# Optimization experiments

Measured on AMD Instinct MI355X. Metric: run time of the kernel, lower is better.

Reference implementation:

```python
import math
import jax, jax.numpy as jnp
import numpy as np

B, S, D, H, HD = 32, 512, 768, 12, 64
K, ST = 2, 2  # pooling kernel / stride
NEG = jnp.float32(-10000.0)


def _alibi_slopes(n):
    def p2(m):
        start = 2 ** (-(2 ** (-(math.log2(m) - 3))))
        return [start * start ** i for i in range(m)]
    if math.log2(n).is_integer():
        return p2(n)
    c = 2 ** math.floor(math.log2(n))
    return p2(c) + _alibi_slopes(2 * c)[0::2][: n - c]


def _sum_pool(x, k, s, out_len):
    # x: [B, L, C]; ceil_mode sum-pool over axis 1 (zero padded on the right)
    pad = (out_len - 1) * s + k - x.shape[1]
    if pad > 0:
        x = jnp.pad(x, ((0, 0), (0, pad), (0, 0)))
    win = x[:, jnp.arange(out_len)[:, None] * s + jnp.arange(k)]  # [B, out, k, C]
    return win.sum(axis=2)


def setup_inputs() -> dict:
    key = jax.random.key(0)
    k1, k2, k3 = jax.random.split(key, 3)
    hidden_states = jax.random.normal(k1, (B, S, D), dtype=jnp.float32)
    lengths = jax.random.randint(k2, (B,), 128, S + 1)
    attention_mask = jnp.arange(S)[None, :] < lengths[:, None]  # bool [B,S]
    Wqkv_w = jax.random.normal(k3, (3 * D, D), dtype=jnp.float32) * 0.02
    Wqkv_b = jnp.zeros((3 * D,), dtype=jnp.float32)
    return {"hidden_states": hidden_states, "attention_mask": attention_mask,
            "Wqkv_w": Wqkv_w, "Wqkv_b": Wqkv_b}


def reference(hidden_states, attention_mask, Wqkv_w, Wqkv_b):
    b, s = attention_mask.shape
    qkv = hidden_states @ Wqkv_w.T + Wqkv_b  # [B,S,3D]
    qkv = qkv.reshape(b, s, 3, H, HD)        # '(t h d)' split order
    q = qkv[:, :, 0]                          # [B,S,H,HD]
    k = qkv[:, :, 1].transpose(0, 2, 1, 3)    # [B,H,S,HD]
    v = qkv[:, :, 2].transpose(0, 2, 1, 3)

    # MaskedAvgPool1d on queries (flattened heads), ceil_mode sum-pool / count
    kk = min(K, s)
    out_len = -(-(max(0, s - kk)) // ST) + 1
    q_flat = q.reshape(b, s, H * HD)
    q_flat = jnp.where(attention_mask[:, :, None], q_flat, 0.0)
    norm = _sum_pool(attention_mask.astype(jnp.float32)[:, :, None], kk, ST, out_len)  # [B,out,1]
    new_mask = norm[..., 0] != 0
    norm = jnp.where(norm == 0, 1.0, norm)
    q_pool = _sum_pool(q_flat, kk, ST, out_len) / norm  # [B,out,D]
    q = q_pool.reshape(b, out_len, H, HD).transpose(0, 2, 1, 3)  # [B,H,out,HD]

    # bias: 0 where (new_mask_q & mask_k), else -10000; plus ALiBi
    pair = new_mask[:, :, None] & attention_mask[:, None, :]  # [B,out,S]
    bias = jnp.where(pair, 0.0, NEG)[:, None, :, :]           # [B,1,out,S]
    rel = jnp.abs(jnp.arange(s)[None, :] - jnp.arange(out_len)[:, None])  # [out,S]
    slopes = jnp.asarray(_alibi_slopes(H), dtype=jnp.float32)
    alibi = slopes[:, None, None] * (-rel.astype(jnp.float32))  # [H,out,S]
    scores = jnp.einsum('bhqd,bhkd->bhqk', q, k) / math.sqrt(HD) + bias + alibi[None]
    attn = jax.nn.softmax(scores, axis=-1)
    out = jnp.einsum('bhqk,bhkd->bhqd', attn, v)  # [B,H,out,HD]
    out = out.transpose(0, 2, 1, 3).reshape(b, out_len, H * HD)
    return out, new_mask
```

## Files before the change

kernel.cpp:

```cpp
#include <hip/hip_runtime.h>

#define BB 32
#define SS 512
#define DD 768
#define HH 12
#define HDIM 64
#define OL 256
#define NQKV 2304
#define GM (BB*SS)

#define NEG2 (-14426.9504089f)

typedef __bf16 bf16_t;
typedef bf16_t bf16x8 __attribute__((ext_vector_type(8)));
typedef float f32x4 __attribute__((ext_vector_type(4)));
typedef unsigned short u16x8 __attribute__((ext_vector_type(8)));

__device__ __forceinline__ unsigned short f2bf(float f) {
  unsigned u = __float_as_uint(f);
  u = u + 0x7FFFu + ((u >> 16) & 1u);
  return (unsigned short)(u >> 16);
}
__device__ __forceinline__ float b2f(unsigned short s) {
  return __uint_as_float(((unsigned)s) << 16);
}

__global__ void conv_f32_bf16(const float* __restrict__ in,
                              unsigned short* __restrict__ out, int n4) {
  int i = blockIdx.x * blockDim.x + threadIdx.x;
  if (i >= n4) return;
  float4 v = ((const float4*)in)[i];
  ushort4 o;
  o.x = f2bf(v.x); o.y = f2bf(v.y); o.z = f2bf(v.z); o.w = f2bf(v.w);
  ((ushort4*)out)[i] = o;
}

__global__ void prep_mask(const void* __restrict__ mraw,
                          float* __restrict__ kbias,
                          float* __restrict__ invn,
                          unsigned char* __restrict__ nmask,
                          float* __restrict__ out_nm) {
  int b = blockIdx.x, t = threadIdx.x;
  const unsigned char* mb = (const unsigned char*)mraw;
  bool isbyte = (mb[1] != 0);
  int idx = b * SS + t;
  int mv = isbyte ? (int)(mb[idx] != 0) : (int)(((const int*)mraw)[idx] != 0);
  kbias[idx] = mv ? 0.f : NEG2;
  if (t < OL) {
    int i0 = b * SS + 2 * t, i1 = i0 + 1;
    int m0 = isbyte ? (int)(mb[i0] != 0) : (int)(((const int*)mraw)[i0] != 0);
    int m1 = isbyte ? (int)(mb[i1] != 0) : (int)(((const int*)mraw)[i1] != 0);
    int n = m0 + m1;
    invn[b * OL + t] = (n > 0) ? 1.f / (float)n : 1.f;
    nmask[b * OL + t] = (n > 0) ? 1 : 0;
    out_nm[b * OL + t] = (n > 0) ? 1.f : 0.f;
  }
}

__global__ __launch_bounds__(512, 2) void gemm_qkv(
    const unsigned short* __restrict__ A,
    const unsigned short* __restrict__ Bt,
    const float* __restrict__ bias,
    unsigned short* __restrict__ Kbuf,
    unsigned short* __restrict__ qp,
    unsigned short* __restrict__ vT,
    const float* __restrict__ kbias,
    const float* __restrict__ invn) {
  __shared__ __align__(16) char smem[147456];

  const int t = threadIdx.x;
  const int lane = t & 63;
  const int w = t >> 6;
  const int wm = w >> 2;
  const int wn = w & 3;
  const int fr = lane & 15, hi = lane >> 4;

  const int p = blockIdx.x;
  const int l = (p & 7) * 144 + (p >> 3);
  const int m0 = (l / 9) * 128;
  const int n0 = (l % 9) * 256;
  const int b = m0 >> 9;
  const int s0 = m0 & 511;

  f32x4 acc[4][4] = {};

  const int sr8 = lane >> 3;
  const int sx8 = ((lane & 7) ^ sr8) * 8;
  const int wq = __builtin_amdgcn_readfirstlane(w);
  const unsigned short* aS = A + (size_t)(m0 + wq * 16 + sr8) * DD + sx8;
  const unsigned short* bS = Bt + (size_t)(n0 + wq * 32 + sr8) * DD + sx8;

#define GLOAD(SRC, DST)                                                        \
  __builtin_amdgcn_global_load_lds(                                           \
      (const __attribute__((address_space(1))) unsigned int*)(SRC),           \
      (__attribute__((address_space(3))) unsigned int*)(DST), 16, 0, 0)

#define STG_A(KT, SB, Q) GLOAD(aS + (size_t)(8 * (Q)) * DD + (KT) * 64,        \
                               (SB) + (wq * 16 + 8 * (Q)) * 128)
#define STG_B(KT, SB, Q) GLOAD(bS + (size_t)(8 * (Q)) * DD + (KT) * 64,        \
                               (SB) + 16384 + (wq * 32 + 8 * (Q)) * 128)
#define STG_H1(KT, SB) do { STG_A(KT, SB, 0); STG_A(KT, SB, 1); STG_B(KT, SB, 0); } while (0)
#define STG_H2(KT, SB) do { STG_B(KT, SB, 1); STG_B(KT, SB, 2); STG_B(KT, SB, 3); } while (0)

#define SBAR()                                                                 \
  do {                                                                         \
    __builtin_amdgcn_sched_barrier(0);                                         \
    __builtin_amdgcn_s_barrier();                                              \
    __builtin_amdgcn_sched_barrier(0);                                         \
  } while (0)

#define MFMA16(AF, BF)                                                         \
  do {                                                                         \
    asm volatile("s_waitcnt lgkmcnt(0)" ::: "memory");                          \
    __builtin_amdgcn_sched_barrier(0);                                         \
    __builtin_amdgcn_s_setprio(1);                                             \
    _Pragma("unroll")                                                          \
    for (int mf_ = 0; mf_ < 4; ++mf_)                                          \
      _Pragma("unroll")                                                        \
      for (int nf_ = 0; nf_ < 4; ++nf_)                                        \
        acc[mf_][nf_] = __builtin_amdgcn_mfma_f32_16x16x32_bf16(               \
            (AF)[mf_], (BF)[nf_], acc[mf_][nf_], 0, 0, 0);                     \
    __builtin_amdgcn_s_setprio(0);                                             \
  } while (0)

  const int cb0 = (hi * 16) ^ ((fr & 7) << 4);
  const int cb1 = (64 + hi * 16) ^ ((fr & 7) << 4);
  const int arow = (wm * 64 + fr) * 128;
  const int brow = 16384 + (wn * 64 + fr) * 128;

  STG_H1(0, smem); STG_H2(0, smem);
  STG_H1(1, smem + 49152); STG_H2(1, smem + 49152);

  int se = 0;
#pragma unroll
  for (int it = 0; it < 6; ++it) {
    char* sE = smem + se * 49152;
    char* sO = smem + (se == 2 ? 0 : se + 1) * 49152;
    char* dE = smem + (se == 0 ? 2 : se - 1) * 49152;
    char* dO = sE;
    const int ke = 2 * it + 2, ko = 2 * it + 3;

    bf16x8 af[4], bf[4];

    asm volatile("s_waitcnt vmcnt(6)" ::: "memory");
    SBAR();
#pragma unroll
    for (int f = 0; f < 4; ++f) af[f] = *(const bf16x8*)(sE + arow + f * 2048 + cb0);
#pragma unroll
    for (int f = 0; f < 4; ++f) bf[f] = *(const bf16x8*)(sE + brow + f * 2048 + cb0);
    if (it < 5) STG_H1(ke, dE);
    MFMA16(af, bf);

    SBAR();
#pragma unroll
    for (int f = 0; f < 4; ++f) af[f] = *(const bf16x8*)(sE + arow + f * 2048 + cb1);
#pragma unroll
    for (int f = 0; f < 4; ++f) bf[f] = *(const bf16x8*)(sE + brow + f * 2048 + cb1);
    if (it < 5) STG_H2(ke, dE);
    MFMA16(af, bf);

    if (it < 5) {
      asm volatile("s_waitcnt vmcnt(6)" ::: "memory");
    } else {
      asm volatile("s_waitcnt vmcnt(0)" ::: "memory");
    }
    SBAR();
#pragma unroll
    for (int f = 0; f < 4; ++f) af[f] = *(const bf16x8*)(sO + arow + f * 2048 + cb0);
#pragma unroll
    for (int f = 0; f < 4; ++f) bf[f] = *(const bf16x8*)(sO + brow + f * 2048 + cb0);
    if (it < 5) STG_H1(ko, dO);
    MFMA16(af, bf);

    SBAR();
#pragma unroll
    for (int f = 0; f < 4; ++f) af[f] = *(const bf16x8*)(sO + arow + f * 2048 + cb1);
#pragma unroll
    for (int f = 0; f < 4; ++f) bf[f] = *(const bf16x8*)(sO + brow + f * 2048 + cb1);
    if (it < 5) STG_H2(ko, dO);
    MFMA16(af, bf);

    se = (se + 2) % 3;
  }
#undef STG_A
#undef STG_B
#undef STG_H1
#undef STG_H2
#undef MFMA16
#undef SBAR
#undef GLOAD

  const int nt = n0 / 768;
  if (nt == 1) {
#pragma unroll
    for (int nf = 0; nf < 4; ++nf) {
      const int nc = wn * 64 + nf * 16 + fr;
      const float bvs = bias[n0 + nc];
      const int gnc = n0 - 768 + nc;
#pragma unroll
      for (int mf = 0; mf < 4; ++mf) {
        const int gmr = m0 + wm * 64 + mf * 16 + hi * 4;
#pragma unroll
        for (int j = 0; j < 4; ++j)
          Kbuf[(size_t)(gmr + j) * 768 + gnc] = f2bf(acc[mf][nf][j] + bvs);
      }
    }
  } else if (nt == 0) {
#pragma unroll
    for (int mf = 0; mf < 4; ++mf) {
      const int sl = s0 + wm * 64 + mf * 16 + hi * 4;
      const float4 km = *(const float4*)&kbias[b * SS + sl];
      const float2 iv = *(const float2*)&invn[b * OL + (sl >> 1)];
      const float w0 = (km.x == 0.f) ? iv.x : 0.f;
      const float w1 = (km.y == 0.f) ? iv.x : 0.f;
      const float w2 = (km.z == 0.f) ? iv.y : 0.f;
      const float w3 = (km.w == 0.f) ? iv.y : 0.f;
      const int o0 = b * OL + (sl >> 1);
#pragma unroll
      for (int nf = 0; nf < 4; ++nf) {
        const int gnc = n0 + wn * 64 + nf * 16 + fr;
        const float bvs = bias[gnc];
        const f32x4 a = acc[mf][nf];
        qp[(size_t)o0 * DD + gnc] = f2bf((a[0] + bvs) * w0 + (a[1] + bvs) * w1);
        qp[(size_t)(o0 + 1) * DD + gnc] = f2bf((a[2] + bvs) * w2 + (a[3] + bvs) * w3);
      }
    }
  } else {
    unsigned short* lt = (unsigned short*)smem;
#pragma unroll
    for (int nf = 0; nf < 4; ++nf) {
      const int nl = wn * 64 + nf * 16 + fr;
      const float bvs = bias[n0 + nl];
#pragma unroll
      for (int mf = 0; mf < 4; ++mf) {
        const int ml = wm * 64 + mf * 16 + hi * 4;
        ushort4 pk;
        pk.x = f2bf(acc[mf][nf][0] + bvs);
        pk.y = f2bf(acc[mf][nf][1] + bvs);
        pk.z = f2bf(acc[mf][nf][2] + bvs);
        pk.w = f2bf(acc[mf][nf][3] + bvs);
        *(ushort4*)&lt[nl * 136 + ml] = pk;
      }
    }
    __syncthreads();
#pragma unroll
    for (int i = 0; i < 8; ++i) {
      const int task = i * 512 + t;
      const int r = task >> 4;
      const int ch = task & 15;
      const u16x8 v = *(const u16x8*)&lt[r * 136 + ch * 8];
      const int nv = n0 - 1536 + r;
      const int h2 = nv >> 6, d2 = nv & 63;
      *(u16x8*)(vT + ((size_t)((b * HH + h2) * HDIM + d2)) * 512 + s0 + ch * 8) = v;
    }
  }
}

__constant__ float c_slopes2[12] = {
    0.72134752f, 0.36067376f, 0.18033688f, 0.09016844f,
    0.04508422f, 0.02254211f, 0.011271055f, 0.0056355275f,
    1.02013945f, 0.51006972f, 0.25503486f, 0.12751743f};

__global__ __launch_bounds__(256) void attn_mfma(
    const unsigned short* __restrict__ qp,
    const unsigned short* __restrict__ Kb,
    const unsigned short* __restrict__ vT,
    const float* __restrict__ kbias,
    const unsigned char* __restrict__ nmask,
    float* __restrict__ out) {
  __shared__ __align__(16) char smem[51200];
  const int t = threadIdx.x;
  const int lane = t & 63;
  const int w = t >> 6;
  const int wq = __builtin_amdgcn_readfirstlane(w);
  const int fr = lane & 15, hi = lane >> 4;

  const int p = blockIdx.x;
  const int l = (p & 7) * 96 + (p >> 3);
  const int qb = l & 1;
  const int bh = l >> 1;
  const int h = bh % HH, b = bh / HH;
  const int q0 = qb * 128 + wq * 32;

  char* ptb = smem + 32768 + wq * 4096;
  float* kbl = (float*)(smem + 49152);

  const int srow = lane >> 3;
  const int scol = ((lane & 7) ^ srow) * 8;

#define GLOAD(SRC, DST)                                                        \
  __builtin_amdgcn_global_load_lds(                                           \
      (const __attribute__((address_space(1))) unsigned int*)(SRC),           \
      (__attribute__((address_space(3))) unsigned int*)(DST), 16, 0, 0)

  if (wq == 0) {
    GLOAD(kbias + b * SS + lane * 4, smem + 49152);
    GLOAD(kbias + b * SS + 256 + lane * 4, smem + 50176);
  }

  bf16x8 qf[2][2];
#pragma unroll
  for (int m = 0; m < 2; ++m)
#pragma unroll
    for (int ks = 0; ks < 2; ++ks)
      qf[m][ks] = *(const bf16x8*)(qp + (size_t)(b * OL + q0 + m * 16 + fr) * DD +
                                   h * HDIM + ks * 32 + hi * 8);

  int nmv = (int)nmask[b * OL + q0 + (lane & 31)];
  int qmbits = 0;
#pragma unroll
  for (int m = 0; m < 2; ++m)
#pragma unroll
    for (int j = 0; j < 4; ++j)
      if (__shfl(nmv, m * 16 + hi * 4 + j, 64)) qmbits |= 1 << (m * 4 + j);

  const float slope2 = c_slopes2[h];
  f32x4 oacc[2][4] = {};
  float lpart[2][4] = {};

#define STAGE(TILE, BUF) do {                                                  \
    char* kd_ = smem + (BUF) * 8192 + wq * 2048;                               \
    char* vd_ = smem + 16384 + (BUF) * 8192 + wq * 2048;                       \
    const unsigned short* ks_ =                                                \
        Kb + (size_t)(b * SS + (TILE) * 64 + wq * 16 + srow) * 768 + h * HDIM + scol; \
    const unsigned short* vs_ =                                                \
        vT + (size_t)((b * HH + h) * HDIM + wq * 16 + srow) * SS + (TILE) * 64 + scol; \
    GLOAD(ks_, kd_);                                                           \
    GLOAD(ks_ + (size_t)8 * 768, kd_ + 1024);                                  \
    GLOAD(vs_, vd_);                                                           \
    GLOAD(vs_ + (size_t)8 * SS, vd_ + 1024);                                   \
  } while (0)

  __builtin_amdgcn_sched_barrier(0);
  STAGE(0, 0);
  STAGE(1, 1);
  __builtin_amdgcn_sched_barrier(0);

  for (int tile = 0; tile < 8; ++tile) {
    const int cur = tile & 1;
    const int key0 = tile * 64;
    if (tile < 7) {
      asm volatile("s_waitcnt vmcnt(4)" ::: "memory");
    } else {
      asm volatile("s_waitcnt vmcnt(0)" ::: "memory");
    }
    __builtin_amdgcn_sched_barrier(0);
    __builtin_amdgcn_s_barrier();
    __builtin_amdgcn_sched_barrier(0);

    char* ktb = smem + cur * 8192;
    char* vtb = smem + 16384 + cur * 8192;

    f32x4 sacc[2][4] = {};
#pragma unroll
    for (int ks = 0; ks < 2; ++ks) {
      bf16x8 kf[4];
#pragma unroll
      for (int n = 0; n < 4; ++n) {
        const int by = ((n * 16 + fr) * 128 + (ks * 64 + hi * 16)) ^ ((fr & 7) << 4);
        kf[n] = *(const bf16x8*)(ktb + by);
      }
#pragma unroll
      for (int m = 0; m < 2; ++m)
#pragma unroll
        for (int n = 0; n < 4; ++n)
          sacc[m][n] = __builtin_amdgcn_mfma_f32_16x16x32_bf16(qf[m][ks], kf[n], sacc[m][n], 0, 0, 0);
    }

    float kbv[4], keyfv[4];
#pragma unroll
    for (int n = 0; n < 4; ++n) {
      kbv[n] = kbl[key0 + n * 16 + fr];
      keyfv[n] = (float)(key0 + n * 16 + fr);
    }
#pragma unroll
    for (int m = 0; m < 2; ++m) {
#pragma unroll
      for (int j = 0; j < 4; ++j) {
        const bool qm = (qmbits >> (m * 4 + j)) & 1;
        const float qvf = (float)(q0 + m * 16 + hi * 4 + j);
        float lp = lpart[m][j];
#pragma unroll
        for (int n = 0; n < 4; ++n) {
          const float biasv = qm ? kbv[n] : 0.f;
          const float rel = fabsf(keyfv[n] - qvf);
          float tv = fmaf(sacc[m][n][j], 0.18033688011f, biasv);
          tv = fmaf(rel, -slope2, tv);
          float pe;
          asm("v_exp_f32 %0, %1" : "=v"(pe) : "v"(tv));
          lp += pe;
          const int by = ((m * 16 + hi * 4 + j) * 128 + (n * 16 + fr) * 2) ^
                         (((hi * 4 + j) & 7) << 4);
          *(unsigned short*)(ptb + by) = f2bf(pe);
        }
        lpart[m][j] = lp;
      }
    }
    asm volatile("s_waitcnt lgkmcnt(0)" ::: "memory");
    __builtin_amdgcn_sched_barrier(0);

#pragma unroll
    for (int ks = 0; ks < 2; ++ks) {
      bf16x8 pf[2], vf[4];
#pragma unroll
      for (int m = 0; m < 2; ++m) {
        const int by = ((m * 16 + fr) * 128 + (ks * 64 + hi * 16)) ^ ((fr & 7) << 4);
        pf[m] = *(const bf16x8*)(ptb + by);
      }
#pragma unroll
      for (int nd = 0; nd < 4; ++nd) {
        const int by = ((nd * 16 + fr) * 128 + (ks * 64 + hi * 16)) ^ ((fr & 7) << 4);
        vf[nd] = *(const bf16x8*)(vtb + by);
      }
#pragma unroll
      for (int m = 0; m < 2; ++m)
#pragma unroll
        for (int nd = 0; nd < 4; ++nd)
          oacc[m][nd] = __builtin_amdgcn_mfma_f32_16x16x32_bf16(pf[m], vf[nd], oacc[m][nd], 0, 0, 0);
    }

    __builtin_amdgcn_sched_barrier(0);
    __builtin_amdgcn_s_barrier();
    __builtin_amdgcn_sched_barrier(0);
    if (tile + 2 < 8) STAGE(tile + 2, cur);
  }
#undef STAGE
#undef GLOAD

  float* ot = (float*)(smem + wq * 8704);
#pragma unroll
  for (int m = 0; m < 2; ++m)
#pragma unroll
    for (int j = 0; j < 4; ++j) {
      float lv = lpart[m][j];
      lv += __shfl_xor(lv, 1, 64);
      lv += __shfl_xor(lv, 2, 64);
      lv += __shfl_xor(lv, 4, 64);
      lv += __shfl_xor(lv, 8, 64);
      const float rl = 1.f / lv;
      const int row = m * 16 + hi * 4 + j;
#pragma unroll
      for (int nd = 0; nd < 4; ++nd)
        ot[row * 68 + nd * 16 + fr] = oacc[m][nd][j] * rl;
    }
  asm volatile("s_waitcnt lgkmcnt(0)" ::: "memory");
  __builtin_amdgcn_sched_barrier(0);
#pragma unroll
  for (int i = 0; i < 8; ++i) {
    const int idx = i * 64 + lane;
    const int row = idx >> 4, c4 = idx & 15;
    const float4 v = *(const float4*)&ot[row * 68 + c4 * 4];
    *(float4*)(out + (size_t)(b * OL + q0 + row) * DD + h * HDIM + c4 * 4) = v;
  }
}

extern "C" void kernel_launch(void* const* d_in, const int* in_sizes, int n_in,
                              void* d_out, int out_size, void* d_ws, size_t ws_size,
                              hipStream_t stream) {
  const float* hidden = (const float*)d_in[0];
  const void* maskraw = d_in[1];
  const float* W = (const float*)d_in[2];
  const float* bias = (const float*)d_in[3];
  float* out = (float*)d_out;

  char* ws = (char*)d_ws;
  unsigned short* Abf  = (unsigned short*)(ws);
  unsigned short* Btb  = (unsigned short*)(ws + 25165824);
  unsigned short* Kbuf = (unsigned short*)(ws + 28704768);
  unsigned short* vT   = (unsigned short*)(ws + 53870592);
  unsigned short* qp   = (unsigned short*)(ws + 79036416);
  float* kbias         = (float*)(ws + 91619328);
  float* invn          = (float*)(ws + 91684864);
  unsigned char* nmask = (unsigned char*)(ws + 91717632);

  float* out_nm = out + (size_t)BB * OL * DD;

  conv_f32_bf16<<<(GM * DD / 4 + 255) / 256, 256, 0, stream>>>(hidden, Abf, GM * DD / 4);
  conv_f32_bf16<<<(NQKV * DD / 4 + 255) / 256, 256, 0, stream>>>(W, Btb, NQKV * DD / 4);
  prep_mask<<<BB, SS, 0, stream>>>(maskraw, kbias, invn, nmask, out_nm);
  gemm_qkv<<<1152, 512, 0, stream>>>(Abf, Btb, bias, Kbuf, qp, vT, kbias, invn);
  attn_mfma<<<768, 256, 0, stream>>>(qp, Kbuf, vT, kbias, nmask, out);
}
```

Baseline: 114.8 us.

## Reorder GEMM phases so barrier sits between LDS reads and MFMAs

Restructures the QKV GEMM main loop so each phase issues its LDS fragment reads and global-to-LDS prefetch, then barriers, then runs its MFMAs. The explicit lgkmcnt(0) wait before the MFMAs is removed, so the compiler places the waits itself. The vmcnt waits move to just before the barrier, and a barrier is added after the prologue. Launch bounds drop to one block per CU, loosening register limits at the cost of occupancy. LDS reads now overlap the barrier wait, but correctness depends on the reorder still ordering buffer reuse correctly.

```diff
diff --git a/kernel.cpp b/kernel.cpp
--- a/kernel.cpp
+++ b/kernel.cpp
@@ -57,7 +57,7 @@
   }
 }
 
-__global__ __launch_bounds__(512, 2) void gemm_qkv(
+__global__ __launch_bounds__(512, 1) void gemm_qkv(
     const unsigned short* __restrict__ A,
     const unsigned short* __restrict__ Bt,
     const float* __restrict__ bias,
@@ -102,24 +102,32 @@
 #define STG_H1(KT, SB) do { STG_A(KT, SB, 0); STG_A(KT, SB, 1); STG_B(KT, SB, 0); } while (0)
 #define STG_H2(KT, SB) do { STG_B(KT, SB, 1); STG_B(KT, SB, 2); STG_B(KT, SB, 3); } while (0)
 
-#define SBAR()                                                                 \
+#define RD(SB, CB)                                                             \
+  do {                                                                         \
+    _Pragma("unroll")                                                          \
+    for (int f_ = 0; f_ < 4; ++f_)                                             \
+      af[f_] = *(const bf16x8*)((SB) + arow + f_ * 2048 + (CB));               \
+    _Pragma("unroll")                                                          \
+    for (int f_ = 0; f_ < 4; ++f_)                                             \
+      bf[f_] = *(const bf16x8*)((SB) + brow + f_ * 2048 + (CB));               \
+  } while (0)
+
+#define PHASE_SYNC()                                                           \
   do {                                                                         \
     __builtin_amdgcn_sched_barrier(0);                                         \
     __builtin_amdgcn_s_barrier();                                              \
     __builtin_amdgcn_sched_barrier(0);                                         \
   } while (0)
 
-#define MFMA16(AF, BF)                                                         \
+#define MFMA16()                                                               \
   do {                                                                         \
-    asm volatile("s_waitcnt lgkmcnt(0)" ::: "memory");                          \
-    __builtin_amdgcn_sched_barrier(0);                                         \
     __builtin_amdgcn_s_setprio(1);                                             \
     _Pragma("unroll")                                                          \
     for (int mf_ = 0; mf_ < 4; ++mf_)                                          \
       _Pragma("unroll")                                                        \
       for (int nf_ = 0; nf_ < 4; ++nf_)                                        \
         acc[mf_][nf_] = __builtin_amdgcn_mfma_f32_16x16x32_bf16(               \
-            (AF)[mf_], (BF)[nf_], acc[mf_][nf_], 0, 0, 0);                     \
+            af[mf_], bf[nf_], acc[mf_][nf_], 0, 0, 0);                         \
     __builtin_amdgcn_s_setprio(0);                                             \
   } while (0)
 
@@ -130,6 +138,8 @@
 
   STG_H1(0, smem); STG_H2(0, smem);
   STG_H1(1, smem + 49152); STG_H2(1, smem + 49152);
+  asm volatile("s_waitcnt vmcnt(6)" ::: "memory");
+  PHASE_SYNC();
 
   int se = 0;
 #pragma unroll
@@ -142,43 +152,33 @@
 
     bf16x8 af[4], bf[4];
 
-    asm volatile("s_waitcnt vmcnt(6)" ::: "memory");
-    SBAR();
-#pragma unroll
-    for (int f = 0; f < 4; ++f) af[f] = *(const bf16x8*)(sE + arow + f * 2048 + cb0);
-#pragma unroll
-    for (int f = 0; f < 4; ++f) bf[f] = *(const bf16x8*)(sE + brow + f * 2048 + cb0);
+    RD(sE, cb0);
     if (it < 5) STG_H1(ke, dE);
-    MFMA16(af, bf);
-
-    SBAR();
-#pragma unroll
-    for (int f = 0; f < 4; ++f) af[f] = *(const bf16x8*)(sE + arow + f * 2048 + cb1);
-#pragma unroll
-    for (int f = 0; f < 4; ++f) bf[f] = *(const bf16x8*)(sE + brow + f * 2048 + cb1);
-    if (it < 5) STG_H2(ke, dE);
-    MFMA16(af, bf);
-
+    PHASE_SYNC();
+    MFMA16();
+
+    RD(sE, cb1);
     if (it < 5) {
+      STG_H2(ke, dE);
       asm volatile("s_waitcnt vmcnt(6)" ::: "memory");
     } else {
       asm volatile("s_waitcnt vmcnt(0)" ::: "memory");
     }
-    SBAR();
-#pragma unroll
-    for (int f = 0; f < 4; ++f) af[f] = *(const bf16x8*)(sO + arow + f * 2048 + cb0);
-#pragma unroll
-    for (int f = 0; f < 4; ++f) bf[f] = *(const bf16x8*)(sO + brow + f * 2048 + cb0);
+    PHASE_SYNC();
+    MFMA16();
+
+    RD(sO, cb0);
     if (it < 5) STG_H1(ko, dO);
-    MFMA16(af, bf);
-
-    SBAR();
-#pragma unroll
-    for (int f = 0; f < 4; ++f) af[f] = *(const bf16x8*)(sO + arow + f * 2048 + cb1);
-#pragma unroll
-    for (int f = 0; f < 4; ++f) bf[f] = *(const bf16x8*)(sO + brow + f * 2048 + cb1);
-    if (it < 5) STG_H2(ko, dO);
-    MFMA16(af, bf);
+    PHASE_SYNC();
+    MFMA16();
+
+    RD(sO, cb1);
+    if (it < 5) {
+      STG_H2(ko, dO);
+      asm volatile("s_waitcnt vmcnt(6)" ::: "memory");
+    }
+    PHASE_SYNC();
+    MFMA16();
 
     se = (se + 2) % 3;
   }
@@ -186,8 +186,9 @@
 #undef STG_B
 #undef STG_H1
 #undef STG_H2
+#undef RD
 #undef MFMA16
-#undef SBAR
+#undef PHASE_SYNC
 #undef GLOAD
 
   const int nt = n0 / 768;
```

After: 112.9 us. Within noise of the previous version (-1.7%).
